# Performance work log

Measured on AMD Instinct MI355X. Metric: run time of the kernel, lower is better.

The kernel has to match this reference:

```python
import jax, jax.numpy as jnp
import numpy as np

B, K, D, H, ZDIM = 65536, 16, 64, 128, 16

def setup_inputs() -> dict:
    key = jax.random.key(0)
    ks = jax.random.split(key, 20)
    s = 0.05
    inp = {
        'z': jax.random.normal(ks[0], (B, ZDIM), dtype=jnp.float32),
        'y': jax.random.randint(ks[1], (B,), 0, K),
        # backbone: 4 fc blocks (Linear+ReLU)
        'bw0': jax.random.normal(ks[2], (ZDIM, H), dtype=jnp.float32) * s,
        'bb0': jnp.zeros((H,), dtype=jnp.float32),
        'bw1': jax.random.normal(ks[3], (H, H), dtype=jnp.float32) * s,
        'bb1': jnp.zeros((H,), dtype=jnp.float32),
        'bw2': jax.random.normal(ks[4], (H, H), dtype=jnp.float32) * s,
        'bb2': jnp.zeros((H,), dtype=jnp.float32),
        'bw3': jax.random.normal(ks[5], (H, H), dtype=jnp.float32) * s,
        'bb3': jnp.zeros((H,), dtype=jnp.float32),
        # K heads, weights stacked on leading expert axis; layers 0-2 have ReLU, layer 3 does not
        'hw0': jax.random.normal(ks[6], (K, H, H), dtype=jnp.float32) * s,
        'hb0': jnp.zeros((K, H), dtype=jnp.float32),
        'hw1': jax.random.normal(ks[7], (K, H, H), dtype=jnp.float32) * s,
        'hb1': jnp.zeros((K, H), dtype=jnp.float32),
        'hw2': jax.random.normal(ks[8], (K, H, H), dtype=jnp.float32) * s,
        'hb2': jnp.zeros((K, H), dtype=jnp.float32),
        'hw3': jax.random.normal(ks[9], (K, H, D), dtype=jnp.float32) * s,
        'hb3': jnp.zeros((K, D), dtype=jnp.float32),
    }
    return inp

def reference(z, y, bw0, bb0, bw1, bb1, bw2, bb2, bw3, bb3,
              hw0, hb0, hw1, hb1, hw2, hb2, hw3, hb3):
    h = jax.nn.relu(z @ bw0 + bb0)
    h = jax.nn.relu(h @ bw1 + bb1)
    h = jax.nn.relu(h @ bw2 + bb2)
    h = jax.nn.relu(h @ bw3 + bb3)          # [B, H]
    # all K expert heads (faithful to original: compute all, then gather)
    a = jax.nn.relu(jnp.einsum('bi,kij->bkj', h, hw0) + hb0)  # [B, K, H]
    a = jax.nn.relu(jnp.einsum('bki,kij->bkj', a, hw1) + hb1)
    a = jax.nn.relu(jnp.einsum('bki,kij->bkj', a, hw2) + hb2)
    a = jnp.einsum('bki,kij->bkj', a, hw3) + hb3              # [B, K, D], no ReLU
    # select the y-th head per sample
    out = jnp.take_along_axis(a, y[:, None, None], axis=1)[:, 0, :]  # [B, D]
    return out
```

## Files before the change

### kernel.cpp

```cpp
#include <hip/hip_runtime.h>
#include <hip/hip_bf16.h>
#include <stdint.h>


typedef _Float16 f16;
typedef __attribute__((ext_vector_type(4)))  _Float16 f16x4;
typedef __attribute__((ext_vector_type(8)))  _Float16 f16x8;
typedef __attribute__((ext_vector_type(16))) float    f32x16;
typedef uint32_t u32;

#define MFMA(a, b, c) __builtin_amdgcn_mfma_f32_32x32x16_f16((a), (b), (c), 0, 0, 0)

constexpr int Bc = 65536;
constexpr int Kc = 16;
constexpr int Hc = 128;
constexpr int Dc = 64;

constexpr int CAP  = 4608;
constexpr int BPE  = CAP / 64;
constexpr int NBLK = Kc * BPE;

constexpr float INV_LOSCALE = 1.0f / 1024.0f;

constexpr int BBW_F16 = 2048 + 3 * 16384;
constexpr int HWE_F16 = 3 * 16384 + 8192;

constexpr int PREP_BLKS = 52 + Kc * 56;

__device__ __forceinline__ f32x16 zero16() {
    f32x16 z;
#pragma unroll
    for (int i = 0; i < 16; ++i) z[i] = 0.0f;
    return z;
}

__device__ __forceinline__ int actOff(int s, int u) {
    return s * 128 + ((u ^ (s & 15)) << 3);
}

template<bool RELU>
__device__ __forceinline__ void epi_store(
    const f32x16& aH0, const f32x16& aL0,
    const f32x16& aH1, const f32x16& aL1,
    const float* biasLds, f16* aOut, int wid, int l31, int bh)
{
#pragma unroll
    for (int rg = 0; rg < 4; ++rg) {
        const float4 bv = *(const float4*)(biasLds + 32 * wid + 8 * rg + 4 * bh);
        const float bb[4] = {bv.x, bv.y, bv.z, bv.w};
#pragma unroll
        for (int mt = 0; mt < 2; ++mt) {
            const f32x16& aH = mt ? aH1 : aH0;
            const f32x16& aL = mt ? aL1 : aL0;
            f16x4 h4;
#pragma unroll
            for (int j = 0; j < 4; ++j) {
                float v = fmaf(aL[4 * rg + j], INV_LOSCALE, aH[4 * rg + j]) + bb[j];
                if (RELU) v = fmaxf(v, 0.0f);
                h4[j] = (f16)v;
            }
            const int s = 32 * mt + l31;
            *(f16x4*)(aOut + actOff(s, 4 * wid + rg) + 4 * bh) = h4;
        }
    }
}

__device__ __forceinline__ void layer4(
    const f16* __restrict__ Wh, const f16* __restrict__ Wl,
    const float* biasLds, const f16* aIn, f16* aOut,
    int wid, int lane, int l31, int bh)
{
    const f16* ph = Wh + wid * 4096 + lane * 8;
    const f16* pl = Wl + wid * 4096 + lane * 8;

    f32x16 aH0 = zero16(), aH1 = zero16(), aL0 = zero16(), aL1 = zero16();
#pragma unroll
    for (int ks = 0; ks < 8; ++ks) {
        const f16x8 whi = *(const f16x8*)(ph + ks * 512);
        const f16x8 wlo = *(const f16x8*)(pl + ks * 512);
        const f16x8 a0 = *(const f16x8*)(aIn + actOff(l31,      2 * ks + bh));
        const f16x8 a1 = *(const f16x8*)(aIn + actOff(32 + l31, 2 * ks + bh));
        aH0 = MFMA(whi, a0, aH0);
        aH1 = MFMA(whi, a1, aH1);
        aL0 = MFMA(wlo, a0, aL0);
        aL1 = MFMA(wlo, a1, aL1);
    }
    epi_store<true>(aH0, aL0, aH1, aL1, biasLds, aOut, wid, l31, bh);
}

__global__ __launch_bounds__(256, 3) void fused_mlp(
    const float* __restrict__ z,
    const int* __restrict__ idxb, const int* __restrict__ cursor,
    const f16* __restrict__ bbH, const f16* __restrict__ bbL,
    const float* __restrict__ bb0, const float* __restrict__ bb1,
    const float* __restrict__ bb2, const float* __restrict__ bb3,
    const f16* __restrict__ hH, const f16* __restrict__ hL,
    const float* __restrict__ hb0, const float* __restrict__ hb1,
    const float* __restrict__ hb2, const float* __restrict__ hb3,
    float* __restrict__ out)
{
    __shared__ __attribute__((aligned(16))) f16 A[64 * 128];
    __shared__ __attribute__((aligned(16))) f16 B[64 * 128];
    __shared__ __attribute__((aligned(16))) float BIAS[960];
    __shared__ int sidx[64];

    const int blk = blockIdx.x;
    const int e = blk / BPE;
    const int local0 = (blk % BPE) * 64;
    const int cnt = min(cursor[e * 16], CAP);
    const int nvalid = cnt - local0;
    if (nvalid <= 0) return;

    const int tid = threadIdx.x;
    const int wid = tid >> 6, lane = tid & 63;
    const int l31 = lane & 31, bh = lane >> 5;

#pragma unroll
    for (int r = 0; r < 4; ++r) {
        const int i = r * 256 + tid;
        if (i < 960) {
            float v;
            if      (i < 128) v = bb0[i];
            else if (i < 256) v = bb1[i - 128];
            else if (i < 384) v = bb2[i - 256];
            else if (i < 512) v = bb3[i - 384];
            else if (i < 640) v = hb0[e * Hc + i - 512];
            else if (i < 768) v = hb1[e * Hc + i - 640];
            else if (i < 896) v = hb2[e * Hc + i - 768];
            else              v = hb3[e * Dc + i - 896];
            BIAS[i] = v;
        }
    }
    if (tid < 64) sidx[tid] = (tid < nvalid) ? idxb[e * CAP + local0 + tid] : -1;
    __syncthreads();

    {
        const int m = tid >> 2, q = tid & 3;
        const int b = sidx[m];
        f16x4 t;
        if (b >= 0) {
            const float4 v = *(const float4*)(z + (size_t)b * 16 + q * 4);
            t[0] = (f16)v.x; t[1] = (f16)v.y; t[2] = (f16)v.z; t[3] = (f16)v.w;
        } else {
            t[0] = t[1] = t[2] = t[3] = (f16)0.0f;
        }
        *(f16x4*)(A + actOff(m, q >> 1) + (q & 1) * 4) = t;
    }
    __syncthreads();

    {
        const f16x8 w0h = *(const f16x8*)(bbH + wid * 512 + lane * 8);
        const f16x8 w0l = *(const f16x8*)(bbL + wid * 512 + lane * 8);
        const f16x8 a0 = *(const f16x8*)(A + actOff(l31,      bh));
        const f16x8 a1 = *(const f16x8*)(A + actOff(32 + l31, bh));
        f32x16 aH0 = zero16(), aH1 = zero16(), aL0 = zero16(), aL1 = zero16();
        aH0 = MFMA(w0h, a0, aH0);
        aH1 = MFMA(w0h, a1, aH1);
        aL0 = MFMA(w0l, a0, aL0);
        aL1 = MFMA(w0l, a1, aL1);
        epi_store<true>(aH0, aL0, aH1, aL1, BIAS, B, wid, l31, bh);
    }
    __syncthreads();

    layer4(bbH + 2048,  bbL + 2048,  BIAS + 128, B, A, wid, lane, l31, bh);
    __syncthreads();
    layer4(bbH + 18432, bbL + 18432, BIAS + 256, A, B, wid, lane, l31, bh);
    __syncthreads();
    layer4(bbH + 34816, bbL + 34816, BIAS + 384, B, A, wid, lane, l31, bh);
    __syncthreads();

    const size_t we = (size_t)e * HWE_F16;
    layer4(hH + we,         hL + we,         BIAS + 512, A, B, wid, lane, l31, bh);
    __syncthreads();
    layer4(hH + we + 16384, hL + we + 16384, BIAS + 640, B, A, wid, lane, l31, bh);
    __syncthreads();
    layer4(hH + we + 32768, hL + we + 32768, BIAS + 768, A, B, wid, lane, l31, bh);
    __syncthreads();

    if (wid < 2) {
        const f16* ph = hH + we + 49152 + wid * 4096 + lane * 8;
        const f16* pl = hL + we + 49152 + wid * 4096 + lane * 8;
        f32x16 aH0 = zero16(), aH1 = zero16(), aL0 = zero16(), aL1 = zero16();
#pragma unroll
        for (int ks = 0; ks < 8; ++ks) {
            const f16x8 whi = *(const f16x8*)(ph + ks * 512);
            const f16x8 wlo = *(const f16x8*)(pl + ks * 512);
            const f16x8 a0 = *(const f16x8*)(B + actOff(l31,      2 * ks + bh));
            const f16x8 a1 = *(const f16x8*)(B + actOff(32 + l31, 2 * ks + bh));
            aH0 = MFMA(whi, a0, aH0);
            aH1 = MFMA(whi, a1, aH1);
            aL0 = MFMA(wlo, a0, aL0);
            aL1 = MFMA(wlo, a1, aL1);
        }
#pragma unroll
        for (int mt = 0; mt < 2; ++mt) {
            const int b = sidx[32 * mt + l31];
            if (b < 0) continue;
            const f32x16& aH = mt ? aH1 : aH0;
            const f32x16& aL = mt ? aL1 : aL0;
#pragma unroll
            for (int rg = 0; rg < 4; ++rg) {
                const int nb = 32 * wid + 8 * rg + 4 * bh;
                const float4 bv = *(const float4*)(BIAS + 896 + nb);
                float4 v;
                v.x = fmaf(aL[4 * rg + 0], INV_LOSCALE, aH[4 * rg + 0]) + bv.x;
                v.y = fmaf(aL[4 * rg + 1], INV_LOSCALE, aH[4 * rg + 1]) + bv.y;
                v.z = fmaf(aL[4 * rg + 2], INV_LOSCALE, aH[4 * rg + 2]) + bv.z;
                v.w = fmaf(aL[4 * rg + 3], INV_LOSCALE, aH[4 * rg + 3]) + bv.w;
                *(float4*)(out + (size_t)b * Dc + nb) = v;
            }
        }
    }
}

__global__ void prep_scatter(
    const float* __restrict__ bw0, const float* __restrict__ bw1,
    const float* __restrict__ bw2, const float* __restrict__ bw3,
    const float* __restrict__ hw0, const float* __restrict__ hw1,
    const float* __restrict__ hw2, const float* __restrict__ hw3,
    f16* __restrict__ bbH, f16* __restrict__ bbL,
    f16* __restrict__ hH,  f16* __restrict__ hL,
    const int* __restrict__ y, int* __restrict__ idxb, int* __restrict__ cursor)
{
    __shared__ float T[32][33];
    __shared__ int lc[Kc];
    __shared__ int lbase[Kc];
    const int id = blockIdx.x;
    const int tx = threadIdx.x;

    if (id >= PREP_BLKS) {
        if (tx < Kc) lc[tx] = 0;
        __syncthreads();
        const int b = (id - PREP_BLKS) * 256 + tx;
        const int e = y[b];
        const int r = atomicAdd(&lc[e], 1);
        __syncthreads();
        if (tx < Kc) lbase[tx] = atomicAdd(&cursor[tx * 16], lc[tx]);
        __syncthreads();
        const int slot = lbase[e] + r;
        if (slot < CAP) idxb[e * CAP + slot] = b;
        return;
    }

    const float* src; f16 *dh, *dl;
    int K, N, k0, n0;
    bool big;

    if (id < 52) {
        if (id < 4) {
            src = bw0; dh = bbH; dl = bbL;
            K = 16; N = 128; k0 = 0; n0 = id * 32; big = false;
        } else {
            const int t = id - 4;
            const int l = t / 16, tile = t % 16;
            const float* bws[3] = {bw1, bw2, bw3};
            src = bws[l];
            dh = bbH + 2048 + l * 16384;
            dl = bbL + 2048 + l * 16384;
            K = 128; N = 128; big = true;
            k0 = (tile >> 2) * 32; n0 = (tile & 3) * 32;
        }
    } else {
        const int t = id - 52;
        const int e = t / 56, r = t % 56;
        if (r < 48) {
            const int l = r / 16, tile = r % 16;
            const float* hws[3] = {hw0, hw1, hw2};
            src = hws[l] + (size_t)e * 16384;
            dh = hH + (size_t)e * HWE_F16 + l * 16384;
            dl = hL + (size_t)e * HWE_F16 + l * 16384;
            K = 128; N = 128; big = true;
            k0 = (tile >> 2) * 32; n0 = (tile & 3) * 32;
        } else {
            const int r2 = r - 48;
            src = hw3 + (size_t)e * 8192;
            dh = hH + (size_t)e * HWE_F16 + 49152;
            dl = hL + (size_t)e * HWE_F16 + 49152;
            K = 128; N = 64; big = true;
            k0 = (r2 >> 1) * 32; n0 = (r2 & 1) * 32;
        }
    }

    const int c = tx & 31, g = tx >> 5;
#pragma unroll
    for (int i = 0; i < 4; ++i) {
        const int row = g * 4 + i;
        if (k0 + row < K)
            T[c][row] = src[(size_t)(k0 + row) * N + n0 + c];
    }
    __syncthreads();
#pragma unroll
    for (int i = 0; i < 4; ++i) {
        const int n = n0 + g * 4 + i;
        const int k = k0 + c;
        if (k < K) {
            const float v = T[g * 4 + i][c];
            const f16 hi = (f16)v;
            const f16 lo = (f16)((v - (float)hi) * 1024.0f);
            size_t didx;
            if (big)
                didx = (size_t)(n >> 5) * 4096 + (size_t)(k >> 4) * 512
                     + ((k >> 3) & 1) * 256 + (n & 31) * 8 + (k & 7);
            else
                didx = (size_t)(n >> 5) * 512 + (size_t)(k >> 3) * 256
                     + (n & 31) * 8 + (k & 7);
            dh[didx] = hi;
            dl[didx] = lo;
        }
    }
}

extern "C" void kernel_launch(void* const* d_in, const int* in_sizes, int n_in,
                              void* d_out, int out_size, void* d_ws, size_t ws_size,
                              hipStream_t stream)
{
    const float* z   = (const float*)d_in[0];
    const int*   y   = (const int*)d_in[1];
    const float* bw0 = (const float*)d_in[2];
    const float* bb0 = (const float*)d_in[3];
    const float* bw1 = (const float*)d_in[4];
    const float* bb1 = (const float*)d_in[5];
    const float* bw2 = (const float*)d_in[6];
    const float* bb2 = (const float*)d_in[7];
    const float* bw3 = (const float*)d_in[8];
    const float* bb3 = (const float*)d_in[9];
    const float* hw0 = (const float*)d_in[10];
    const float* hb0 = (const float*)d_in[11];
    const float* hw1 = (const float*)d_in[12];
    const float* hb1 = (const float*)d_in[13];
    const float* hw2 = (const float*)d_in[14];
    const float* hb2 = (const float*)d_in[15];
    const float* hw3 = (const float*)d_in[16];
    const float* hb3 = (const float*)d_in[17];
    float* out = (float*)d_out;

    char* p = (char*)d_ws;
    f16* bbH = (f16*)p;  p += (size_t)BBW_F16 * 2;
    f16* bbL = (f16*)p;  p += (size_t)BBW_F16 * 2;
    f16* hH  = (f16*)p;  p += (size_t)Kc * HWE_F16 * 2;
    f16* hL  = (f16*)p;  p += (size_t)Kc * HWE_F16 * 2;
    int* idxb = (int*)p; p += (size_t)Kc * CAP * 4;
    int* cursor = (int*)p;

    hipMemsetAsync(cursor, 0, 256 * sizeof(int), stream);

    prep_scatter<<<PREP_BLKS + Bc / 256, 256, 0, stream>>>(
        bw0, bw1, bw2, bw3, hw0, hw1, hw2, hw3,
        bbH, bbL, hH, hL, y, idxb, cursor);

    fused_mlp<<<NBLK, 256, 0, stream>>>(
        z, idxb, cursor, bbH, bbL, bb0, bb1, bb2, bb3,
        hH, hL, hb0, hb1, hb2, hb3, out);
}
```

Before: 151.3 us.

## Convert fused MLP to persistent kernel with atomic work-stealing tile queue

```diff
diff --git a/kernel.cpp b/kernel.cpp
--- a/kernel.cpp
+++ b/kernel.cpp
@@ -18,7 +18,8 @@
 
 constexpr int CAP  = 4608;
 constexpr int BPE  = CAP / 64;
-constexpr int NBLK = Kc * BPE;
+constexpr int NTILE = Kc * BPE;
+constexpr int PGRID = 1024;
 
 constexpr float INV_LOSCALE = 1.0f / 1024.0f;
 
@@ -91,6 +92,7 @@
 __global__ __launch_bounds__(256, 3) void fused_mlp(
     const float* __restrict__ z,
     const int* __restrict__ idxb, const int* __restrict__ cursor,
+    int* __restrict__ workctr,
     const f16* __restrict__ bbH, const f16* __restrict__ bbL,
     const float* __restrict__ bb0, const float* __restrict__ bb1,
     const float* __restrict__ bb2, const float* __restrict__ bb3,
@@ -103,111 +105,119 @@
     __shared__ __attribute__((aligned(16))) f16 B[64 * 128];
     __shared__ __attribute__((aligned(16))) float BIAS[960];
     __shared__ int sidx[64];
-
-    const int blk = blockIdx.x;
-    const int e = blk / BPE;
-    const int local0 = (blk % BPE) * 64;
-    const int cnt = min(cursor[e * 16], CAP);
-    const int nvalid = cnt - local0;
-    if (nvalid <= 0) return;
+    __shared__ int stile;
 
     const int tid = threadIdx.x;
     const int wid = tid >> 6, lane = tid & 63;
     const int l31 = lane & 31, bh = lane >> 5;
 
-#pragma unroll
-    for (int r = 0; r < 4; ++r) {
-        const int i = r * 256 + tid;
-        if (i < 960) {
-            float v;
-            if      (i < 128) v = bb0[i];
-            else if (i < 256) v = bb1[i - 128];
-            else if (i < 384) v = bb2[i - 256];
-            else if (i < 512) v = bb3[i - 384];
-            else if (i < 640) v = hb0[e * Hc + i - 512];
-            else if (i < 768) v = hb1[e * Hc + i - 640];
-            else if (i < 896) v = hb2[e * Hc + i - 768];
-            else              v = hb3[e * Dc + i - 896];
-            BIAS[i] = v;
-        }
-    }
-    if (tid < 64) sidx[tid] = (tid < nvalid) ? idxb[e * CAP + local0 + tid] : -1;
-    __syncthreads();
-
-    {
-        const int m = tid >> 2, q = tid & 3;
-        const int b = sidx[m];
-        f16x4 t;
-        if (b >= 0) {
-            const float4 v = *(const float4*)(z + (size_t)b * 16 + q * 4);
-            t[0] = (f16)v.x; t[1] = (f16)v.y; t[2] = (f16)v.z; t[3] = (f16)v.w;
-        } else {
-            t[0] = t[1] = t[2] = t[3] = (f16)0.0f;
-        }
-        *(f16x4*)(A + actOff(m, q >> 1) + (q & 1) * 4) = t;
-    }
-    __syncthreads();
-
-    {
-        const f16x8 w0h = *(const f16x8*)(bbH + wid * 512 + lane * 8);
-        const f16x8 w0l = *(const f16x8*)(bbL + wid * 512 + lane * 8);
-        const f16x8 a0 = *(const f16x8*)(A + actOff(l31,      bh));
-        const f16x8 a1 = *(const f16x8*)(A + actOff(32 + l31, bh));
-        f32x16 aH0 = zero16(), aH1 = zero16(), aL0 = zero16(), aL1 = zero16();
-        aH0 = MFMA(w0h, a0, aH0);
-        aH1 = MFMA(w0h, a1, aH1);
-        aL0 = MFMA(w0l, a0, aL0);
-        aL1 = MFMA(w0l, a1, aL1);
-        epi_store<true>(aH0, aL0, aH1, aL1, BIAS, B, wid, l31, bh);
-    }
-    __syncthreads();
-
-    layer4(bbH + 2048,  bbL + 2048,  BIAS + 128, B, A, wid, lane, l31, bh);
-    __syncthreads();
-    layer4(bbH + 18432, bbL + 18432, BIAS + 256, A, B, wid, lane, l31, bh);
-    __syncthreads();
-    layer4(bbH + 34816, bbL + 34816, BIAS + 384, B, A, wid, lane, l31, bh);
-    __syncthreads();
-
-    const size_t we = (size_t)e * HWE_F16;
-    layer4(hH + we,         hL + we,         BIAS + 512, A, B, wid, lane, l31, bh);
-    __syncthreads();
-    layer4(hH + we + 16384, hL + we + 16384, BIAS + 640, B, A, wid, lane, l31, bh);
-    __syncthreads();
-    layer4(hH + we + 32768, hL + we + 32768, BIAS + 768, A, B, wid, lane, l31, bh);
-    __syncthreads();
-
-    if (wid < 2) {
-        const f16* ph = hH + we + 49152 + wid * 4096 + lane * 8;
-        const f16* pl = hL + we + 49152 + wid * 4096 + lane * 8;
-        f32x16 aH0 = zero16(), aH1 = zero16(), aL0 = zero16(), aL1 = zero16();
-#pragma unroll
-        for (int ks = 0; ks < 8; ++ks) {
-            const f16x8 whi = *(const f16x8*)(ph + ks * 512);
-            const f16x8 wlo = *(const f16x8*)(pl + ks * 512);
-            const f16x8 a0 = *(const f16x8*)(B + actOff(l31,      2 * ks + bh));
-            const f16x8 a1 = *(const f16x8*)(B + actOff(32 + l31, 2 * ks + bh));
-            aH0 = MFMA(whi, a0, aH0);
-            aH1 = MFMA(whi, a1, aH1);
-            aL0 = MFMA(wlo, a0, aL0);
-            aL1 = MFMA(wlo, a1, aL1);
-        }
-#pragma unroll
-        for (int mt = 0; mt < 2; ++mt) {
-            const int b = sidx[32 * mt + l31];
-            if (b < 0) continue;
-            const f32x16& aH = mt ? aH1 : aH0;
-            const f32x16& aL = mt ? aL1 : aL0;
-#pragma unroll
-            for (int rg = 0; rg < 4; ++rg) {
-                const int nb = 32 * wid + 8 * rg + 4 * bh;
-                const float4 bv = *(const float4*)(BIAS + 896 + nb);
-                float4 v;
-                v.x = fmaf(aL[4 * rg + 0], INV_LOSCALE, aH[4 * rg + 0]) + bv.x;
-                v.y = fmaf(aL[4 * rg + 1], INV_LOSCALE, aH[4 * rg + 1]) + bv.y;
-                v.z = fmaf(aL[4 * rg + 2], INV_LOSCALE, aH[4 * rg + 2]) + bv.z;
-                v.w = fmaf(aL[4 * rg + 3], INV_LOSCALE, aH[4 * rg + 3]) + bv.w;
-                *(float4*)(out + (size_t)b * Dc + nb) = v;
+    for (;;) {
+        __syncthreads();
+        if (tid == 0) stile = atomicAdd(workctr, 1);
+        __syncthreads();
+        const int t = stile;
+        if (t >= NTILE) return;
+
+        const int e = t / BPE;
+        const int local0 = (t % BPE) * 64;
+        const int cnt = min(cursor[e * 16], CAP);
+        const int nvalid = cnt - local0;
+        if (nvalid <= 0) continue;
+
+#pragma unroll
+        for (int r = 0; r < 4; ++r) {
+            const int i = r * 256 + tid;
+            if (i < 960) {
+                float v;
+                if      (i < 128) v = bb0[i];
+                else if (i < 256) v = bb1[i - 128];
+                else if (i < 384) v = bb2[i - 256];
+                else if (i < 512) v = bb3[i - 384];
+                else if (i < 640) v = hb0[e * Hc + i - 512];
+                else if (i < 768) v = hb1[e * Hc + i - 640];
+                else if (i < 896) v = hb2[e * Hc + i - 768];
+                else              v = hb3[e * Dc + i - 896];
+                BIAS[i] = v;
+            }
+        }
+        if (tid < 64) sidx[tid] = (tid < nvalid) ? idxb[e * CAP + local0 + tid] : -1;
+        __syncthreads();
+
+        {
+            const int m = tid >> 2, q = tid & 3;
+            const int b = sidx[m];
+            f16x4 tt;
+            if (b >= 0) {
+                const float4 v = *(const float4*)(z + (size_t)b * 16 + q * 4);
+                tt[0] = (f16)v.x; tt[1] = (f16)v.y; tt[2] = (f16)v.z; tt[3] = (f16)v.w;
+            } else {
+                tt[0] = tt[1] = tt[2] = tt[3] = (f16)0.0f;
+            }
+            *(f16x4*)(A + actOff(m, q >> 1) + (q & 1) * 4) = tt;
+        }
+        __syncthreads();
+
+        {
+            const f16x8 w0h = *(const f16x8*)(bbH + wid * 512 + lane * 8);
+            const f16x8 w0l = *(const f16x8*)(bbL + wid * 512 + lane * 8);
+            const f16x8 a0 = *(const f16x8*)(A + actOff(l31,      bh));
+            const f16x8 a1 = *(const f16x8*)(A + actOff(32 + l31, bh));
+            f32x16 aH0 = zero16(), aH1 = zero16(), aL0 = zero16(), aL1 = zero16();
+            aH0 = MFMA(w0h, a0, aH0);
+            aH1 = MFMA(w0h, a1, aH1);
+            aL0 = MFMA(w0l, a0, aL0);
+            aL1 = MFMA(w0l, a1, aL1);
+            epi_store<true>(aH0, aL0, aH1, aL1, BIAS, B, wid, l31, bh);
+        }
+        __syncthreads();
+
+        layer4(bbH + 2048,  bbL + 2048,  BIAS + 128, B, A, wid, lane, l31, bh);
+        __syncthreads();
+        layer4(bbH + 18432, bbL + 18432, BIAS + 256, A, B, wid, lane, l31, bh);
+        __syncthreads();
+        layer4(bbH + 34816, bbL + 34816, BIAS + 384, B, A, wid, lane, l31, bh);
+        __syncthreads();
+
+        const size_t we = (size_t)e * HWE_F16;
+        layer4(hH + we,         hL + we,         BIAS + 512, A, B, wid, lane, l31, bh);
+        __syncthreads();
+        layer4(hH + we + 16384, hL + we + 16384, BIAS + 640, B, A, wid, lane, l31, bh);
+        __syncthreads();
+        layer4(hH + we + 32768, hL + we + 32768, BIAS + 768, A, B, wid, lane, l31, bh);
+        __syncthreads();
+
+        if (wid < 2) {
+            const f16* ph = hH + we + 49152 + wid * 4096 + lane * 8;
+            const f16* pl = hL + we + 49152 + wid * 4096 + lane * 8;
+            f32x16 aH0 = zero16(), aH1 = zero16(), aL0 = zero16(), aL1 = zero16();
+#pragma unroll
+            for (int ks = 0; ks < 8; ++ks) {
+                const f16x8 whi = *(const f16x8*)(ph + ks * 512);
+                const f16x8 wlo = *(const f16x8*)(pl + ks * 512);
+                const f16x8 a0 = *(const f16x8*)(B + actOff(l31,      2 * ks + bh));
+                const f16x8 a1 = *(const f16x8*)(B + actOff(32 + l31, 2 * ks + bh));
+                aH0 = MFMA(whi, a0, aH0);
+                aH1 = MFMA(whi, a1, aH1);
+                aL0 = MFMA(wlo, a0, aL0);
+                aL1 = MFMA(wlo, a1, aL1);
+            }
+#pragma unroll
+            for (int mt = 0; mt < 2; ++mt) {
+                const int b = sidx[32 * mt + l31];
+                if (b < 0) continue;
+                const f32x16& aH = mt ? aH1 : aH0;
+                const f32x16& aL = mt ? aL1 : aL0;
+#pragma unroll
+                for (int rg = 0; rg < 4; ++rg) {
+                    const int nb = 32 * wid + 8 * rg + 4 * bh;
+                    const float4 bv = *(const float4*)(BIAS + 896 + nb);
+                    float4 v;
+                    v.x = fmaf(aL[4 * rg + 0], INV_LOSCALE, aH[4 * rg + 0]) + bv.x;
+                    v.y = fmaf(aL[4 * rg + 1], INV_LOSCALE, aH[4 * rg + 1]) + bv.y;
+                    v.z = fmaf(aL[4 * rg + 2], INV_LOSCALE, aH[4 * rg + 2]) + bv.z;
+                    v.w = fmaf(aL[4 * rg + 3], INV_LOSCALE, aH[4 * rg + 3]) + bv.w;
+                    *(float4*)(out + (size_t)b * Dc + nb) = v;
+                }
             }
         }
     }
@@ -341,14 +351,15 @@
     f16* hL  = (f16*)p;  p += (size_t)Kc * HWE_F16 * 2;
     int* idxb = (int*)p; p += (size_t)Kc * CAP * 4;
     int* cursor = (int*)p;
-
-    hipMemsetAsync(cursor, 0, 256 * sizeof(int), stream);
+    int* workctr = cursor + 256;
+
+    hipMemsetAsync(cursor, 0, 2048, stream);
 
     prep_scatter<<<PREP_BLKS + Bc / 256, 256, 0, stream>>>(
         bw0, bw1, bw2, bw3, hw0, hw1, hw2, hw3,
         bbH, bbL, hH, hL, y, idxb, cursor);
 
-    fused_mlp<<<NBLK, 256, 0, stream>>>(
-        z, idxb, cursor, bbH, bbL, bb0, bb1, bb2, bb3,
+    fused_mlp<<<PGRID, 256, 0, stream>>>(
+        z, idxb, cursor, workctr, bbH, bbL, bb0, bb1, bb2, bb3,
         hH, hL, hb0, hb1, hb2, hb3, out);
 }
```

After: 179.0 us. +18.3%, slower.
